# Kernel optimization log

Measured on AMD Instinct MI355X. Metric: run time of the kernel, lower is better.

Reference implementation:

```python
import jax, jax.numpy as jnp
import numpy as np

N_HEAD, D_MODEL, D_K, D_V = 4, 512, 128, 128
B, LQ, LK = 1024, 32, 64
EPS = 1e-5


def setup_inputs() -> dict:
    key = jax.random.key(0)
    ks = jax.random.split(key, 10)
    s = 0.02
    q = jax.random.normal(ks[0], (B, LQ, D_MODEL), jnp.float32)
    k = jax.random.normal(ks[1], (B, LK, D_MODEL), jnp.float32)
    v = jax.random.normal(ks[2], (B, LK, D_MODEL), jnp.float32)
    mask = jax.random.bernoulli(ks[3], 0.15, (B, LQ, LK))  # True = null neighbor
    Wq = jax.random.normal(ks[4], (N_HEAD * D_K, D_MODEL), jnp.float32) * s
    Wk = jax.random.normal(ks[5], (N_HEAD * D_K, D_MODEL), jnp.float32) * s
    Wv = jax.random.normal(ks[6], (N_HEAD * D_K, D_MODEL), jnp.float32) * s
    Wmap = jax.random.normal(ks[7], (1, 2 * D_K), jnp.float32) * s
    fcW = jax.random.normal(ks[8], (D_MODEL, N_HEAD * D_V), jnp.float32) * s
    fcb = jnp.zeros((D_MODEL,), jnp.float32)
    gamma = jnp.ones((D_MODEL,), jnp.float32)
    beta = jnp.zeros((D_MODEL,), jnp.float32)
    return dict(q=q, k=k, v=v, mask=mask, Wq=Wq, Wk=Wk, Wv=Wv, Wmap=Wmap,
                fcW=fcW, fcb=fcb, gamma=gamma, beta=beta)


def reference(q, k, v, mask, Wq, Wk, Wv, Wmap, fcW, fcb, gamma, beta):
    # Projections -> [B, L, H, d]
    qp = (q @ Wq.T).reshape(B, LQ, N_HEAD, D_K)
    kp = (k @ Wk.T).reshape(B, LK, N_HEAD, D_K)
    vp = (v @ Wv.T).reshape(B, LK, N_HEAD, D_V)
    # weight_map(concat(q,k)) == q . w_left + k . w_right  (exact same math,
    # avoids materializing the expanded [H*B, LQ, LK, 2*D_K] concat tensor)
    wm_q, wm_k = Wmap[0, :D_K], Wmap[0, D_K:]
    sq = jnp.einsum('bqhd,d->hbq', qp, wm_q)  # [H, B, LQ]
    sk = jnp.einsum('bkhd,d->hbk', kp, wm_k)  # [H, B, LK]
    attn = sq[:, :, :, None] + sk[:, :, None, :]  # [H, B, LQ, LK]
    attn = jnp.where(mask[None], jnp.float32(-1e10), attn)
    attn = jax.nn.softmax(attn, axis=-1)
    # dropout is identity (eval / p=0)
    out = jnp.einsum('hbqk,bkhd->bqhd', attn, vp).reshape(B, LQ, N_HEAD * D_V)
    out = jax.nn.leaky_relu(out @ fcW.T + fcb, negative_slope=0.2)
    out = out + q  # residual
    mu = out.mean(-1, keepdims=True)
    var = out.var(-1, keepdims=True)
    out = gamma * (out - mu) / jnp.sqrt(var + EPS) + beta
    return out, attn.reshape(N_HEAD * B, LQ, LK)
```

## Files before the change

### kernel.cpp

```cpp
#include <hip/hip_runtime.h>
#include <hip/hip_bf16.h>

#define NHEAD 4
#define DMODEL 512
#define DK 128
#define BB 1024
#define LQ 32
#define LK 64
#define LN_EPS 1e-5f

typedef __attribute__((ext_vector_type(8))) __bf16 bf16x8;
typedef __attribute__((ext_vector_type(8))) short short8;
typedef __attribute__((ext_vector_type(4))) float floatx4;

__device__ __forceinline__ float b2f(unsigned short u) {
  unsigned v = ((unsigned)u) << 16;
  return __builtin_bit_cast(float, v);
}
__device__ __forceinline__ unsigned short f2b(float f) {
  unsigned u = __builtin_bit_cast(unsigned, f);
  u += 0x7fffu + ((u >> 16) & 1u);
  return (unsigned short)(u >> 16);
}
__device__ __forceinline__ float ldS(const void* p, size_t i, int f32) {
  return f32 ? ((const float*)p)[i] : b2f(((const unsigned short*)p)[i]);
}
__device__ __forceinline__ void load8f(const void* base, size_t i8, int f32, float o[8]) {
  if (f32) {
    const float* p = (const float*)base + i8;
    float4 a = *(const float4*)p, b = *(const float4*)(p + 4);
    o[0] = a.x; o[1] = a.y; o[2] = a.z; o[3] = a.w;
    o[4] = b.x; o[5] = b.y; o[6] = b.z; o[7] = b.w;
  } else {
    short8 v = *(const short8*)((const unsigned short*)base + i8);
#pragma unroll
    for (int j = 0; j < 8; ++j) o[j] = b2f(((const unsigned short*)&v)[j]);
  }
}

__global__ void detect_kernel(const unsigned* __restrict__ gbits,
                              const unsigned* __restrict__ mbits,
                              unsigned* __restrict__ flags) {
  if (threadIdx.x == 0) flags[0] = (gbits[0] == 0x3F800000u) ? 1u : 0u;
  if (threadIdx.x == 1) {
    unsigned any = 0;
    for (int i = 0; i < 64; ++i) {
      unsigned w = mbits[i];
      if (w != 0u && w != 1u && w != 0xFFFFFFFFu) any = 1;
    }
    flags[1] = any;
  }
}
__device__ __forceinline__ int mread(const void* m, size_t i, int m8) {
  return m8 ? (int)((const unsigned char*)m)[i] : (((const int*)m)[i] != 0);
}

__global__ __launch_bounds__(256) void convw_kernel(
    const void* __restrict__ Wv, const void* __restrict__ fcW,
    unsigned short* __restrict__ Wv_c, unsigned short* __restrict__ fcW_c,
    const unsigned* __restrict__ flags) {
  int f32 = flags[0];
  int idx = blockIdx.x * 256 + threadIdx.x;
  int sel = idx >> 15;
  size_t i8 = (size_t)(idx & 32767) * 8;
  float x[8];
  load8f(sel ? fcW : Wv, i8, f32, x);
  unsigned short o[8];
#pragma unroll
  for (int j = 0; j < 8; ++j) o[j] = f2b(x[j]);
  *(short8*)((sel ? fcW_c : Wv_c) + i8) = *(const short8*)o;
}

__global__ __launch_bounds__(256) void prep_weff(
    const void* __restrict__ Wq, const void* __restrict__ Wk,
    const void* __restrict__ Wmap,
    float* __restrict__ wq_eff, float* __restrict__ wk_eff,
    const unsigned* __restrict__ flags) {
  int f32 = flags[0];
  int idx = blockIdx.x * 256 + threadIdx.x;
  int sel = idx >> 11;
  int i = idx & 2047;
  int h = i >> 9, m = i & 511;
  const void* W = sel ? Wk : Wq;
  float acc = 0.f;
  for (int d = 0; d < DK; ++d)
    acc += ldS(W, (size_t)(h * DK + d) * DMODEL + m, f32) * ldS(Wmap, sel * DK + d, f32);
  (sel ? wk_eff : wq_eff)[i] = acc;
}

__global__ __launch_bounds__(256) void sqk_kernel(
    const void* __restrict__ q, const void* __restrict__ k,
    const float* __restrict__ wq_eff, const float* __restrict__ wk_eff,
    float* __restrict__ sq, float* __restrict__ sk,
    const unsigned* __restrict__ flags) {
  int f32 = flags[0];
  __shared__ float weff[2][2048];
  for (int i = threadIdx.x; i < 4096; i += 256)
    (&weff[0][0])[i] = (i < 2048) ? wq_eff[i] : wk_eff[i - 2048];
  __syncthreads();
  int w = threadIdx.x >> 6, lane = threadIdx.x & 63;
  int r = blockIdx.x * 4 + w;
  const void* src; float* dst; const float* we;
  if (r < BB * LQ) {
    src = q; dst = sq + (size_t)r * 4; we = weff[0];
  } else {
    r -= BB * LQ;
    src = k; dst = sk + (size_t)r * 4; we = weff[1];
  }
  float x[8];
  load8f(src, (size_t)r * DMODEL + lane * 8, f32, x);
  float acc[4];
#pragma unroll
  for (int h = 0; h < 4; ++h) {
    float a = 0.f;
#pragma unroll
    for (int j = 0; j < 8; ++j) a += x[j] * we[h * 512 + lane * 8 + j];
    acc[h] = a;
  }
#pragma unroll
  for (int h = 0; h < 4; ++h)
#pragma unroll
    for (int off = 32; off; off >>= 1) acc[h] += __shfl_xor(acc[h], off, 64);
  if (lane == 0) { dst[0] = acc[0]; dst[1] = acc[1]; dst[2] = acc[2]; dst[3] = acc[3]; }
}

__global__ __launch_bounds__(512, 2) void fused_kernel(
    const void* __restrict__ v, const unsigned short* __restrict__ Wv_c,
    const unsigned short* __restrict__ fcW_c,
    const float* __restrict__ sq, const float* __restrict__ sk,
    const void* __restrict__ mask, const void* __restrict__ qin,
    const void* __restrict__ fcb, const void* __restrict__ gamma,
    const void* __restrict__ beta, void* __restrict__ d_out,
    const unsigned* __restrict__ flags) {
  int f32 = flags[0], m8 = flags[1];
  int b = blockIdx.x;
  __shared__ short vps[64][520];
  __shared__ short att[32][520];
  __shared__ float sqs[4][32], sks[4][64];
  __shared__ float pr[8][64];
  __shared__ float gbb[3][512];
  __shared__ float psum[8][32], psum2[8][32];
  __shared__ float rmu[32], rinv[32];
  int tid = threadIdx.x;
  int wv = tid >> 6, lane = tid & 63, l16 = lane & 15, quad = lane >> 4;

  for (int i = tid; i < 4096; i += 512) {
    int e = i * 8, row = e >> 9, col = e & 511;
    float x[8];
    load8f(v, (size_t)b * (64 * 512) + e, f32, x);
    unsigned short o[8];
#pragma unroll
    for (int j = 0; j < 8; ++j) o[j] = f2b(x[j]);
    *(short8*)&vps[row][col] = *(const short8*)o;
  }
  for (int i = tid; i < 1536; i += 512) {
    int arr = i >> 9, j = i & 511;
    const void* p = arr == 0 ? fcb : (arr == 1 ? gamma : beta);
    gbb[arr][j] = ldS(p, j, f32);
  }
  if (tid < 128) sqs[tid >> 5][tid & 31] = sq[(size_t)(b * 32 + (tid & 31)) * 4 + (tid >> 5)];
  else if (tid < 384) {
    int t = tid - 128;
    sks[t >> 6][t & 63] = sk[(size_t)(b * 64 + (t & 63)) * 4 + (t >> 6)];
  }
  __syncthreads();

  floatx4 acc1[4][4] = {};
  for (int k0 = 0; k0 < 512; k0 += 32) {
    bf16x8 af[4], wf[4];
#pragma unroll
    for (int mf = 0; mf < 4; ++mf)
      af[mf] = __builtin_bit_cast(bf16x8, *(const short8*)&vps[mf * 16 + l16][k0 + quad * 8]);
#pragma unroll
    for (int nf = 0; nf < 4; ++nf)
      wf[nf] = __builtin_bit_cast(bf16x8,
          *(const short8*)(Wv_c + (size_t)(wv * 64 + nf * 16 + l16) * 512 + k0 + quad * 8));
#pragma unroll
    for (int mf = 0; mf < 4; ++mf)
#pragma unroll
      for (int nf = 0; nf < 4; ++nf)
        acc1[mf][nf] = __builtin_amdgcn_mfma_f32_16x16x32_bf16(af[mf], wf[nf], acc1[mf][nf], 0, 0, 0);
  }
  __syncthreads();

#pragma unroll
  for (int mf = 0; mf < 4; ++mf)
#pragma unroll
    for (int nf = 0; nf < 4; ++nf)
#pragma unroll
      for (int r = 0; r < 4; ++r)
        vps[mf * 16 + quad * 4 + r][wv * 64 + nf * 16 + l16] = f2b(acc1[mf][nf][r]);
  __syncthreads();

  {
    int h = wv >> 1, qb = (wv & 1) * 16;
    char* abase = (char*)d_out + ((size_t)BB * LQ * DMODEL << (f32 ? 2 : 1));
    for (int i = 0; i < 16; ++i) {
      int qrow = qb + i;
      float s = sqs[h][qrow] + sks[h][lane];
      if (mread(mask, ((size_t)b * 32 + qrow) * 64 + lane, m8)) s = -1e10f;
      float mx = s;
#pragma unroll
      for (int off = 32; off; off >>= 1) mx = fmaxf(mx, __shfl_xor(mx, off, 64));
      float p = __expf(s - mx);
      float sm = p;
#pragma unroll
      for (int off = 32; off; off >>= 1) sm += __shfl_xor(sm, off, 64);
      float pn = p / sm;
      size_t oi = ((size_t)(h * 1024 + b) * 32 + qrow) * 64 + lane;
      if (f32) ((float*)abase)[oi] = pn; else ((unsigned short*)abase)[oi] = f2b(pn);
      pr[wv][lane] = pn;
      float a0 = 0.f, a1 = 0.f;
#pragma unroll
      for (int kk = 0; kk < 64; ++kk) {
        float pk = pr[wv][kk];
        unsigned u = *(const unsigned*)&vps[kk][h * 128 + 2 * lane];
        a0 += pk * b2f((unsigned short)(u & 0xffffu));
        a1 += pk * b2f((unsigned short)(u >> 16));
      }
      *(unsigned*)&att[qrow][h * 128 + 2 * lane] =
          (unsigned)f2b(a0) | ((unsigned)f2b(a1) << 16);
    }
  }
  __syncthreads();

  floatx4 acc2[2][4] = {};
  for (int k0 = 0; k0 < 512; k0 += 32) {
    bf16x8 af2[2], wf2[4];
#pragma unroll
    for (int mf = 0; mf < 2; ++mf)
      af2[mf] = __builtin_bit_cast(bf16x8, *(const short8*)&att[mf * 16 + l16][k0 + quad * 8]);
#pragma unroll
    for (int nf = 0; nf < 4; ++nf)
      wf2[nf] = __builtin_bit_cast(bf16x8,
          *(const short8*)(fcW_c + (size_t)(wv * 64 + nf * 16 + l16) * 512 + k0 + quad * 8));
#pragma unroll
    for (int mf = 0; mf < 2; ++mf)
#pragma unroll
      for (int nf = 0; nf < 4; ++nf)
        acc2[mf][nf] = __builtin_amdgcn_mfma_f32_16x16x32_bf16(af2[mf], wf2[nf], acc2[mf][nf], 0, 0, 0);
  }

#pragma unroll
  for (int mf = 0; mf < 2; ++mf)
#pragma unroll
    for (int r = 0; r < 4; ++r) {
      int rloc = mf * 16 + quad * 4 + r;
      float s = 0.f, s2 = 0.f;
#pragma unroll
      for (int nf = 0; nf < 4; ++nf) {
        int col = wv * 64 + nf * 16 + l16;
        float x = acc2[mf][nf][r] + gbb[0][col];
        x = x > 0.f ? x : 0.2f * x;
        x += ldS(qin, (size_t)(b * 32 + rloc) * 512 + col, f32);
        acc2[mf][nf][r] = x;
        s += x;
        s2 += x * x;
      }
#pragma unroll
      for (int off = 1; off < 16; off <<= 1) {
        s += __shfl_xor(s, off, 64);
        s2 += __shfl_xor(s2, off, 64);
      }
      if (l16 == 0) { psum[wv][rloc] = s; psum2[wv][rloc] = s2; }
    }
  __syncthreads();
  if (tid < 32) {
    float s = 0.f, s2 = 0.f;
#pragma unroll
    for (int w = 0; w < 8; ++w) { s += psum[w][tid]; s2 += psum2[w][tid]; }
    float mu = s * (1.f / 512.f);
    float var = s2 * (1.f / 512.f) - mu * mu;
    rmu[tid] = mu;
    rinv[tid] = rsqrtf(var + LN_EPS);
  }
  __syncthreads();
#pragma unroll
  for (int mf = 0; mf < 2; ++mf)
#pragma unroll
    for (int r = 0; r < 4; ++r) {
      int rloc = mf * 16 + quad * 4 + r;
      float mu = rmu[rloc], inv = rinv[rloc];
#pragma unroll
      for (int nf = 0; nf < 4; ++nf) {
        int col = wv * 64 + nf * 16 + l16;
        float y = gbb[1][col] * (acc2[mf][nf][r] - mu) * inv + gbb[2][col];
        size_t oi = (size_t)(b * 32 + rloc) * 512 + col;
        if (f32) ((float*)d_out)[oi] = y; else ((unsigned short*)d_out)[oi] = f2b(y);
      }
    }
}

extern "C" void kernel_launch(void* const* d_in, const int* in_sizes, int n_in,
                              void* d_out, int out_size, void* d_ws, size_t ws_size,
                              hipStream_t stream) {
  const void* q = d_in[0];
  const void* k = d_in[1];
  const void* v = d_in[2];
  const void* mask = d_in[3];
  const void* Wq = d_in[4];
  const void* Wk = d_in[5];
  const void* Wv = d_in[6];
  const void* Wmap = d_in[7];
  const void* fcW = d_in[8];
  const void* fcb = d_in[9];
  const void* gamma = d_in[10];
  const void* beta = d_in[11];

  char* ws = (char*)d_ws;
  unsigned short* Wv_c = (unsigned short*)ws;
  unsigned short* fcW_c = (unsigned short*)(ws + 524288);
  float* wq_eff = (float*)(ws + 1048576);
  float* wk_eff = (float*)(ws + 1056768);
  float* sqv = (float*)(ws + 1064960);
  float* skv = (float*)(ws + 1589248);
  unsigned* flags = (unsigned*)(ws + 2637824);
  const size_t REQUIRED = 2637888ull;
  if (ws_size < REQUIRED) return;

  detect_kernel<<<1, 64, 0, stream>>>((const unsigned*)gamma, (const unsigned*)mask, flags);
  convw_kernel<<<256, 256, 0, stream>>>(Wv, fcW, Wv_c, fcW_c, flags);
  prep_weff<<<16, 256, 0, stream>>>(Wq, Wk, Wmap, wq_eff, wk_eff, flags);
  sqk_kernel<<<(BB * LQ + BB * LK) / 4, 256, 0, stream>>>(q, k, wq_eff, wk_eff, sqv, skv, flags);
  fused_kernel<<<BB, 512, 0, stream>>>(v, Wv_c, fcW_c, sqv, skv, mask, q, fcb, gamma, beta,
                                       d_out, flags);
}
```

Before: 678.3 us.

## Fuse score projection into main kernel and use MFMA for attention-times-V

Folds the separate sq/sk projection kernel into the fused per-batch kernel, so q and k rows are dotted with the effective weights inside each block and the intermediate sq/sk buffers and one launch disappear. The scalar probability×V loop is replaced by an MFMA bf16 matmul: probabilities are staged in shared memory and the projected V fragments stay in registers, redistributed with cross-lane shuffles. Shared memory is unioned into one buffer and the bias, gamma and beta arrays move to registers, so launch bounds can rise to 4 blocks per CU. In exchange the code adds register pressure and shuffle overhead, and probabilities are now rounded to bf16 before the PV product.

```diff
diff --git a/kernel.cpp b/kernel.cpp
--- a/kernel.cpp
+++ b/kernel.cpp
@@ -12,6 +12,7 @@
 typedef __attribute__((ext_vector_type(8))) __bf16 bf16x8;
 typedef __attribute__((ext_vector_type(8))) short short8;
 typedef __attribute__((ext_vector_type(4))) float floatx4;
+typedef __attribute__((ext_vector_type(4))) unsigned uintx4;
 
 __device__ __forceinline__ float b2f(unsigned short u) {
   unsigned v = ((unsigned)u) << 16;
@@ -88,61 +89,57 @@
   (sel ? wk_eff : wq_eff)[i] = acc;
 }
 
-__global__ __launch_bounds__(256) void sqk_kernel(
-    const void* __restrict__ q, const void* __restrict__ k,
+__global__ __launch_bounds__(512, 4) void fused_kernel(
+    const void* __restrict__ v, const void* __restrict__ qin,
+    const void* __restrict__ kin,
+    const unsigned short* __restrict__ Wv_c,
+    const unsigned short* __restrict__ fcW_c,
     const float* __restrict__ wq_eff, const float* __restrict__ wk_eff,
-    float* __restrict__ sq, float* __restrict__ sk,
-    const unsigned* __restrict__ flags) {
-  int f32 = flags[0];
-  __shared__ float weff[2][2048];
-  for (int i = threadIdx.x; i < 4096; i += 256)
-    (&weff[0][0])[i] = (i < 2048) ? wq_eff[i] : wk_eff[i - 2048];
-  __syncthreads();
-  int w = threadIdx.x >> 6, lane = threadIdx.x & 63;
-  int r = blockIdx.x * 4 + w;
-  const void* src; float* dst; const float* we;
-  if (r < BB * LQ) {
-    src = q; dst = sq + (size_t)r * 4; we = weff[0];
-  } else {
-    r -= BB * LQ;
-    src = k; dst = sk + (size_t)r * 4; we = weff[1];
-  }
-  float x[8];
-  load8f(src, (size_t)r * DMODEL + lane * 8, f32, x);
-  float acc[4];
-#pragma unroll
-  for (int h = 0; h < 4; ++h) {
-    float a = 0.f;
-#pragma unroll
-    for (int j = 0; j < 8; ++j) a += x[j] * we[h * 512 + lane * 8 + j];
-    acc[h] = a;
-  }
-#pragma unroll
-  for (int h = 0; h < 4; ++h)
-#pragma unroll
-    for (int off = 32; off; off >>= 1) acc[h] += __shfl_xor(acc[h], off, 64);
-  if (lane == 0) { dst[0] = acc[0]; dst[1] = acc[1]; dst[2] = acc[2]; dst[3] = acc[3]; }
-}
-
-__global__ __launch_bounds__(512, 2) void fused_kernel(
-    const void* __restrict__ v, const unsigned short* __restrict__ Wv_c,
-    const unsigned short* __restrict__ fcW_c,
-    const float* __restrict__ sq, const float* __restrict__ sk,
-    const void* __restrict__ mask, const void* __restrict__ qin,
+    const void* __restrict__ mask,
     const void* __restrict__ fcb, const void* __restrict__ gamma,
     const void* __restrict__ beta, void* __restrict__ d_out,
     const unsigned* __restrict__ flags) {
   int f32 = flags[0], m8 = flags[1];
   int b = blockIdx.x;
-  __shared__ short vps[64][520];
-  __shared__ short att[32][520];
+  __shared__ __align__(16) short U[64 * 520];
   __shared__ float sqs[4][32], sks[4][64];
-  __shared__ float pr[8][64];
-  __shared__ float gbb[3][512];
   __shared__ float psum[8][32], psum2[8][32];
   __shared__ float rmu[32], rinv[32];
+  short (*vps)[520] = (short(*)[520])U;
+  short (*probs)[72] = (short(*)[72])U;
+  short (*att)[520] = (short(*)[520])U;
   int tid = threadIdx.x;
   int wv = tid >> 6, lane = tid & 63, l16 = lane & 15, quad = lane >> 4;
+
+  {
+#pragma unroll 4
+    for (int rr = 0; rr < 12; ++rr) {
+      int r = wv * 12 + rr;
+      int isq = r < 32;
+      int lr = isq ? r : r - 32;
+      size_t base = isq ? ((size_t)b * 32 + lr) : ((size_t)b * 64 + lr);
+      float x[8];
+      load8f(isq ? qin : kin, base * DMODEL + lane * 8, f32, x);
+      const float* we = (isq ? wq_eff : wk_eff) + lane * 8;
+      float acc[4];
+#pragma unroll
+      for (int h = 0; h < 4; ++h) {
+        const float4* wp = (const float4*)(we + h * 512);
+        float4 wa = wp[0], wb = wp[1];
+        acc[h] = x[0] * wa.x + x[1] * wa.y + x[2] * wa.z + x[3] * wa.w +
+                 x[4] * wb.x + x[5] * wb.y + x[6] * wb.z + x[7] * wb.w;
+      }
+#pragma unroll
+      for (int h = 0; h < 4; ++h)
+#pragma unroll
+        for (int off = 32; off; off >>= 1) acc[h] += __shfl_xor(acc[h], off, 64);
+      if (lane == 0) {
+#pragma unroll
+        for (int h = 0; h < 4; ++h)
+          (isq ? &sqs[h][lr] : &sks[h][lr])[0] = acc[h];
+      }
+    }
+  }
 
   for (int i = tid; i < 4096; i += 512) {
     int e = i * 8, row = e >> 9, col = e & 511;
@@ -153,16 +150,6 @@
     for (int j = 0; j < 8; ++j) o[j] = f2b(x[j]);
     *(short8*)&vps[row][col] = *(const short8*)o;
   }
-  for (int i = tid; i < 1536; i += 512) {
-    int arr = i >> 9, j = i & 511;
-    const void* p = arr == 0 ? fcb : (arr == 1 ? gamma : beta);
-    gbb[arr][j] = ldS(p, j, f32);
-  }
-  if (tid < 128) sqs[tid >> 5][tid & 31] = sq[(size_t)(b * 32 + (tid & 31)) * 4 + (tid >> 5)];
-  else if (tid < 384) {
-    int t = tid - 128;
-    sks[t >> 6][t & 63] = sk[(size_t)(b * 64 + (t & 63)) * 4 + (t >> 6)];
-  }
   __syncthreads();
 
   floatx4 acc1[4][4] = {};
@@ -181,23 +168,24 @@
       for (int nf = 0; nf < 4; ++nf)
         acc1[mf][nf] = __builtin_amdgcn_mfma_f32_16x16x32_bf16(af[mf], wf[nf], acc1[mf][nf], 0, 0, 0);
   }
-  __syncthreads();
-
+  unsigned pk1[4][4][2];
 #pragma unroll
   for (int mf = 0; mf < 4; ++mf)
 #pragma unroll
-    for (int nf = 0; nf < 4; ++nf)
-#pragma unroll
-      for (int r = 0; r < 4; ++r)
-        vps[mf * 16 + quad * 4 + r][wv * 64 + nf * 16 + l16] = f2b(acc1[mf][nf][r]);
-  __syncthreads();
-
+    for (int nf = 0; nf < 4; ++nf) {
+      pk1[mf][nf][0] = (unsigned)f2b(acc1[mf][nf][0]) | ((unsigned)f2b(acc1[mf][nf][1]) << 16);
+      pk1[mf][nf][1] = (unsigned)f2b(acc1[mf][nf][2]) | ((unsigned)f2b(acc1[mf][nf][3]) << 16);
+    }
+  __syncthreads();
+
+  int h = wv >> 1;
   {
-    int h = wv >> 1, qb = (wv & 1) * 16;
+    int qb = (wv & 1) * 16;
     char* abase = (char*)d_out + ((size_t)BB * LQ * DMODEL << (f32 ? 2 : 1));
+    float skl = sks[h][lane];
     for (int i = 0; i < 16; ++i) {
       int qrow = qb + i;
-      float s = sqs[h][qrow] + sks[h][lane];
+      float s = sqs[h][qrow] + skl;
       if (mread(mask, ((size_t)b * 32 + qrow) * 64 + lane, m8)) s = -1e10f;
       float mx = s;
 #pragma unroll
@@ -209,19 +197,57 @@
       float pn = p / sm;
       size_t oi = ((size_t)(h * 1024 + b) * 32 + qrow) * 64 + lane;
       if (f32) ((float*)abase)[oi] = pn; else ((unsigned short*)abase)[oi] = f2b(pn);
-      pr[wv][lane] = pn;
-      float a0 = 0.f, a1 = 0.f;
-#pragma unroll
-      for (int kk = 0; kk < 64; ++kk) {
-        float pk = pr[wv][kk];
-        unsigned u = *(const unsigned*)&vps[kk][h * 128 + 2 * lane];
-        a0 += pk * b2f((unsigned short)(u & 0xffffu));
-        a1 += pk * b2f((unsigned short)(u >> 16));
-      }
-      *(unsigned*)&att[qrow][h * 128 + 2 * lane] =
-          (unsigned)f2b(a0) | ((unsigned)f2b(a1) << 16);
-    }
-  }
+      float pn2 = __shfl_xor(pn, 1, 64);
+      if (!(lane & 1))
+        *(unsigned*)&probs[h * 32 + qrow][lane] =
+            (unsigned)f2b(pn) | ((unsigned)f2b(pn2) << 16);
+    }
+  }
+  __syncthreads();
+
+  floatx4 accp[2][4] = {};
+  {
+    int lo = l16 + ((quad & 1) << 5);
+    int hi = lo + 16;
+    int hiHalf = quad >> 1;
+#pragma unroll
+    for (int ks = 0; ks < 2; ++ks) {
+      bf16x8 pa[2];
+#pragma unroll
+      for (int m2 = 0; m2 < 2; ++m2)
+        pa[m2] = __builtin_bit_cast(bf16x8,
+            *(const short8*)&probs[h * 32 + m2 * 16 + l16][ks * 32 + quad * 8]);
+#pragma unroll
+      for (int nf = 0; nf < 4; ++nf) {
+        unsigned la0 = __shfl(pk1[2 * ks][nf][0], lo, 64);
+        unsigned la1 = __shfl(pk1[2 * ks][nf][1], lo, 64);
+        unsigned ha0 = __shfl(pk1[2 * ks][nf][0], hi, 64);
+        unsigned ha1 = __shfl(pk1[2 * ks][nf][1], hi, 64);
+        unsigned lb0 = __shfl(pk1[2 * ks + 1][nf][0], lo, 64);
+        unsigned lb1 = __shfl(pk1[2 * ks + 1][nf][1], lo, 64);
+        unsigned hb0 = __shfl(pk1[2 * ks + 1][nf][0], hi, 64);
+        unsigned hb1 = __shfl(pk1[2 * ks + 1][nf][1], hi, 64);
+        uintx4 bw;
+        bw.x = hiHalf ? lb0 : la0;
+        bw.y = hiHalf ? lb1 : la1;
+        bw.z = hiHalf ? hb0 : ha0;
+        bw.w = hiHalf ? hb1 : ha1;
+        bf16x8 bfr = __builtin_bit_cast(bf16x8, bw);
+#pragma unroll
+        for (int m2 = 0; m2 < 2; ++m2)
+          accp[m2][nf] = __builtin_amdgcn_mfma_f32_16x16x32_bf16(pa[m2], bfr, accp[m2][nf], 0, 0, 0);
+      }
+    }
+  }
+  __syncthreads();
+
+#pragma unroll
+  for (int m2 = 0; m2 < 2; ++m2)
+#pragma unroll
+    for (int nf = 0; nf < 4; ++nf)
+#pragma unroll
+      for (int r = 0; r < 4; ++r)
+        att[m2 * 16 + quad * 4 + r][wv * 64 + nf * 16 + l16] = f2b(accp[m2][nf][r]);
   __syncthreads();
 
   floatx4 acc2[2][4] = {};
@@ -241,6 +267,14 @@
         acc2[mf][nf] = __builtin_amdgcn_mfma_f32_16x16x32_bf16(af2[mf], wf2[nf], acc2[mf][nf], 0, 0, 0);
   }
 
+  float fcbv[4], gmv[4], btv[4];
+#pragma unroll
+  for (int nf = 0; nf < 4; ++nf) {
+    int col = wv * 64 + nf * 16 + l16;
+    fcbv[nf] = ldS(fcb, col, f32);
+    gmv[nf] = ldS(gamma, col, f32);
+    btv[nf] = ldS(beta, col, f32);
+  }
 #pragma unroll
   for (int mf = 0; mf < 2; ++mf)
 #pragma unroll
@@ -250,7 +284,7 @@
 #pragma unroll
       for (int nf = 0; nf < 4; ++nf) {
         int col = wv * 64 + nf * 16 + l16;
-        float x = acc2[mf][nf][r] + gbb[0][col];
+        float x = acc2[mf][nf][r] + fcbv[nf];
         x = x > 0.f ? x : 0.2f * x;
         x += ldS(qin, (size_t)(b * 32 + rloc) * 512 + col, f32);
         acc2[mf][nf][r] = x;
@@ -284,7 +318,7 @@
 #pragma unroll
       for (int nf = 0; nf < 4; ++nf) {
         int col = wv * 64 + nf * 16 + l16;
-        float y = gbb[1][col] * (acc2[mf][nf][r] - mu) * inv + gbb[2][col];
+        float y = gmv[nf] * (acc2[mf][nf][r] - mu) * inv + btv[nf];
         size_t oi = (size_t)(b * 32 + rloc) * 512 + col;
         if (f32) ((float*)d_out)[oi] = y; else ((unsigned short*)d_out)[oi] = f2b(y);
       }
@@ -312,8 +346,6 @@
   unsigned short* fcW_c = (unsigned short*)(ws + 524288);
   float* wq_eff = (float*)(ws + 1048576);
   float* wk_eff = (float*)(ws + 1056768);
-  float* sqv = (float*)(ws + 1064960);
-  float* skv = (float*)(ws + 1589248);
   unsigned* flags = (unsigned*)(ws + 2637824);
   const size_t REQUIRED = 2637888ull;
   if (ws_size < REQUIRED) return;
@@ -321,7 +353,6 @@
   detect_kernel<<<1, 64, 0, stream>>>((const unsigned*)gamma, (const unsigned*)mask, flags);
   convw_kernel<<<256, 256, 0, stream>>>(Wv, fcW, Wv_c, fcW_c, flags);
   prep_weff<<<16, 256, 0, stream>>>(Wq, Wk, Wmap, wq_eff, wk_eff, flags);
-  sqk_kernel<<<(BB * LQ + BB * LK) / 4, 256, 0, stream>>>(q, k, wq_eff, wk_eff, sqv, skv, flags);
-  fused_kernel<<<BB, 512, 0, stream>>>(v, Wv_c, fcW_c, sqv, skv, mask, q, fcb, gamma, beta,
-                                       d_out, flags);
-}
+  fused_kernel<<<BB, 512, 0, stream>>>(v, q, k, Wv_c, fcW_c, wq_eff, wk_eff, mask,
+                                       fcb, gamma, beta, d_out, flags);
+}
```

Result: faster. 547.8 us (-19.2%).
